# Kernel tuning notes

Hardware: AMD Instinct MI355X
Metric: run time of the kernel (lower is better)

Reference implementation:

```python
import jax, jax.numpy as jnp
import numpy as np

LAPLACE_SCALE = 0.5


def setup_inputs() -> dict:
    key = jax.random.key(0)
    k1, k2, k3 = jax.random.split(key, 3)
    B, M, D = 8, 512, 64
    return {
        "k": jax.random.normal(k1, (B, M, D), dtype=jnp.float32),
        "v": jax.random.normal(k2, (B, M, D), dtype=jnp.float32),
        "q": jax.random.normal(k3, (B, M, D), dtype=jnp.float32),
    }


def reference(k, v, q):
    # Laplace attention branch (faithful to original, including comparing k to v):
    # k_: [B,1,M,D], v_: [B,M,1,D] -> unnorm: [B,M,M]
    unnorm = jnp.abs((k[:, None, :, :] - v[:, :, None, :]) * LAPLACE_SCALE).sum(axis=-1)
    weights = jax.nn.softmax(unnorm, axis=-1)  # [B,M,M]
    rep = jnp.einsum('bik,bkj->bij', weights, v)  # [B,M,D]
    return rep
```

## Files before the change

kernel.cpp:

```cpp
#include <hip/hip_runtime.h>


typedef _Float16 h2 __attribute__((ext_vector_type(2)));

#if __has_builtin(__builtin_amdgcn_fdot2)
#define FDOT2(a, b, c) __builtin_amdgcn_fdot2((a), (b), (c), false)
#else
static __device__ inline float FDOT2(h2 a, h2 b, float c) {
    return c + (float)a.x * (float)b.x + (float)a.y * (float)b.y;
}
#endif

#if __has_builtin(__builtin_amdgcn_sad_u16)
#define SADU16(a, b, c) __builtin_amdgcn_sad_u16((a), (b), (c))
#else
static __device__ inline unsigned SADU16(unsigned a, unsigned b, unsigned c) {
    const unsigned al = a & 0xFFFFu, ah = a >> 16;
    const unsigned bl = b & 0xFFFFu, bh = b >> 16;
    const unsigned dl = al > bl ? al - bl : bl - al;
    const unsigned dh = ah > bh ? ah - bh : bh - ah;
    return c + dl + dh;
}
#endif

static __device__ inline unsigned pk16(float x, float y) {
    h2 h;
    h.x = (_Float16)x;
    h.y = (_Float16)y;
    return __builtin_bit_cast(unsigned, h);
}

static __device__ inline unsigned q16(float x) {
    return (unsigned)(x * 4096.0f + 32768.5f);
}

constexpr int B_ = 8, M_ = 512, D_ = 64;
constexpr int GRID1 = 8 * 16 * 8;
#define C2L  1.761099911e-4f
#define CFIX 67.0f

constexpr int OFF_KH  = 0;
constexpr int OFF_VH  = 2176;
constexpr int OFF_VJ2 = 3328;
constexpr int OFF_WH  = 5504;
constexpr int OFF_DEN = 6528;
constexpr int LDS_U   = 6656;

__global__ __launch_bounds__(256, 4)
void laplace_k1(const float* __restrict__ K, const float* __restrict__ V,
                unsigned* __restrict__ repH, float* __restrict__ den_part) {
    __shared__ __align__(16) unsigned lds[LDS_U];

    const int blk = blockIdx.x;
    const int b  = blk >> 7;
    const int it = (blk >> 3) & 15;
    const int jg = blk & 7;
    const int i0 = it * 32, j0 = jg * 64;

    const float* __restrict__ Kb = K + (size_t)b * (M_ * D_);
    const float* __restrict__ Vb = V + (size_t)b * (M_ * D_);

    const int t = threadIdx.x;

    {
        const int row = t >> 2, dq = t & 3;
        const float* kp = Kb + (size_t)(j0 + row) * D_ + dq * 16;
#pragma unroll
        for (int c = 0; c < 4; ++c) {
            const float4 q = *reinterpret_cast<const float4*>(kp + 4 * c);
            lds[OFF_KH + (dq * 8 + 2 * c + 0) * 68 + row] = q16(q.x) | (q16(q.y) << 16);
            lds[OFF_KH + (dq * 8 + 2 * c + 1) * 68 + row] = q16(q.z) | (q16(q.w) << 16);
        }
    }
    {
        const int row = t >> 3, dq = t & 7;
        const float* vp = Vb + (size_t)(i0 + row) * D_ + dq * 8;
        const float4 a  = *reinterpret_cast<const float4*>(vp);
        const float4 c4 = *reinterpret_cast<const float4*>(vp + 4);
        lds[OFF_VH + (dq * 4 + 0) * 36 + row] = q16(a.x)  | (q16(a.y)  << 16);
        lds[OFF_VH + (dq * 4 + 1) * 36 + row] = q16(a.z)  | (q16(a.w)  << 16);
        lds[OFF_VH + (dq * 4 + 2) * 36 + row] = q16(c4.x) | (q16(c4.y) << 16);
        lds[OFF_VH + (dq * 4 + 3) * 36 + row] = q16(c4.z) | (q16(c4.w) << 16);
    }
    {
        const int j2 = t >> 3;
        const int dc = (t & 7) * 8;
        const float* r0 = Vb + (size_t)(j0 + 2 * j2) * D_ + dc;
        const float* r1 = r0 + D_;
        unsigned o[8];
#pragma unroll
        for (int c = 0; c < 8; c += 4) {
            const float4 a  = *reinterpret_cast<const float4*>(r0 + c);
            const float4 bq = *reinterpret_cast<const float4*>(r1 + c);
            o[c + 0] = pk16(a.x, bq.x);
            o[c + 1] = pk16(a.y, bq.y);
            o[c + 2] = pk16(a.z, bq.z);
            o[c + 3] = pk16(a.w, bq.w);
        }
        *reinterpret_cast<uint4*>(&lds[OFF_VJ2 + j2 * 68 + dc]) =
            make_uint4(o[0], o[1], o[2], o[3]);
        *reinterpret_cast<uint4*>(&lds[OFF_VJ2 + j2 * 68 + dc + 4]) =
            make_uint4(o[4], o[5], o[6], o[7]);
    }
    __syncthreads();

    const int wv = t >> 6, lane = t & 63;
    const int ig = lane >> 2;
    const int jq = lane & 3;

    unsigned sacc[2][4];
#pragma unroll
    for (int a = 0; a < 2; ++a)
#pragma unroll
        for (int c = 0; c < 4; ++c) sacc[a][c] = 0u;

    const unsigned* pV = lds + OFF_VH + ig * 2;
    const unsigned* pK = lds + OFF_KH + wv * 16 + jq * 4;

#pragma unroll 8
    for (int d2 = 0; d2 < 32; ++d2) {
        const uint2 va = *reinterpret_cast<const uint2*>(pV + d2 * 36);
        const uint4 ka = *reinterpret_cast<const uint4*>(pK + d2 * 68);
        sacc[0][0] = SADU16(ka.x, va.x, sacc[0][0]);
        sacc[0][1] = SADU16(ka.y, va.x, sacc[0][1]);
        sacc[0][2] = SADU16(ka.z, va.x, sacc[0][2]);
        sacc[0][3] = SADU16(ka.w, va.x, sacc[0][3]);
        sacc[1][0] = SADU16(ka.x, va.y, sacc[1][0]);
        sacc[1][1] = SADU16(ka.y, va.y, sacc[1][1]);
        sacc[1][2] = SADU16(ka.z, va.y, sacc[1][2]);
        sacc[1][3] = SADU16(ka.w, va.y, sacc[1][3]);
    }

    float w[2][4], den[2];
#pragma unroll
    for (int a = 0; a < 2; ++a) {
        den[a] = 0.f;
#pragma unroll
        for (int c = 0; c < 4; ++c) {
            float e = exp2f((float)sacc[a][c] * C2L - CFIX);
            e = fminf(e, 60000.0f);
            w[a][c] = e;
            den[a] += e;
        }
        den[a] += __shfl_xor(den[a], 1);
        den[a] += __shfl_xor(den[a], 2);
    }
    float* dnl = reinterpret_cast<float*>(lds + OFF_DEN);
    if (jq == 0)
        *reinterpret_cast<float2*>(&dnl[wv * 32 + ig * 2]) = make_float2(den[0], den[1]);

    {
        unsigned* wH = lds + OFF_WH + wv * 256;
        const int j2 = jq * 2;
#pragma unroll
        for (int a = 0; a < 2; ++a) {
            wH[(j2 + 0) * 32 + ig * 2 + a] = pk16(w[a][0], w[a][1]);
            wH[(j2 + 1) * 32 + ig * 2 + a] = pk16(w[a][2], w[a][3]);
        }
    }

    const int ig3 = lane >> 3;
    const int dg  = lane & 7;

    float acc[4][8];
#pragma unroll
    for (int a = 0; a < 4; ++a)
#pragma unroll
        for (int c = 0; c < 8; ++c) acc[a][c] = 0.f;

    const unsigned* pW  = lds + OFF_WH + wv * 256 + ig3 * 4;
    const unsigned* pVJ = lds + OFF_VJ2 + (wv * 8) * 68 + dg * 8;

#pragma unroll
    for (int j2 = 0; j2 < 8; ++j2) {
        const uint4 wq = *reinterpret_cast<const uint4*>(pW + j2 * 32);
        const uint4 v0 = *reinterpret_cast<const uint4*>(pVJ + j2 * 68);
        const uint4 v1 = *reinterpret_cast<const uint4*>(pVJ + j2 * 68 + 4);
        const unsigned wA[4] = {wq.x, wq.y, wq.z, wq.w};
        const unsigned vA[8] = {v0.x, v0.y, v0.z, v0.w, v1.x, v1.y, v1.z, v1.w};
#pragma unroll
        for (int a = 0; a < 4; ++a) {
            const h2 wa = __builtin_bit_cast(h2, wA[a]);
#pragma unroll
            for (int c = 0; c < 8; ++c)
                acc[a][c] = FDOT2(wa, __builtin_bit_cast(h2, vA[c]), acc[a][c]);
        }
    }
    __syncthreads();

    {
        unsigned* cmb = lds + wv * 1024 + lane * 16;
#pragma unroll
        for (int a = 0; a < 4; ++a)
            *reinterpret_cast<uint4*>(cmb + a * 4) =
                make_uint4(pk16(acc[a][0], acc[a][1]), pk16(acc[a][2], acc[a][3]),
                           pk16(acc[a][4], acc[a][5]), pk16(acc[a][6], acc[a][7]));
    }
    __syncthreads();

    {
        const int i_  = t >> 3;
        const int dgr = t & 7;
        const int L   = ((i_ >> 2) << 3) + dgr;
        const int off = (i_ & 3) * 4;

        float x[4] = {0.f, 0.f, 0.f, 0.f}, y[4] = {0.f, 0.f, 0.f, 0.f};
#pragma unroll
        for (int wq = 0; wq < 4; ++wq) {
            const uint4 q = *reinterpret_cast<const uint4*>(lds + wq * 1024 + L * 16 + off);
            const unsigned qa[4] = {q.x, q.y, q.z, q.w};
#pragma unroll
            for (int c = 0; c < 4; ++c) {
                const h2 h = __builtin_bit_cast(h2, qa[c]);
                x[c] += (float)h.x;
                y[c] += (float)h.y;
            }
        }
        *reinterpret_cast<uint4*>(repH + (size_t)blk * 1024 + t * 4) =
            make_uint4(pk16(x[0], y[0]), pk16(x[1], y[1]),
                       pk16(x[2], y[2]), pk16(x[3], y[3]));

        if (t < 32)
            den_part[(size_t)blk * 32 + t] =
                (dnl[t] + dnl[32 + t]) + (dnl[64 + t] + dnl[96 + t]);
    }
}

__global__ __launch_bounds__(256)
void laplace_k2(const unsigned* __restrict__ repH,
                const float* __restrict__ den_part,
                float2* __restrict__ out2) {
    const int gid = blockIdx.x * 256 + threadIdx.x;
    const int b   = gid >> 14;
    const int i9  = (gid >> 5) & 511;
    const int d2  = gid & 31;
    const int it  = i9 >> 5, il = i9 & 31;

    const size_t base = (size_t)(b * 16 + it) * 8;

    float dsum = 0.f;
#pragma unroll
    for (int s = 0; s < 8; ++s) dsum += den_part[(base + s) * 32 + il];

    float ax = 0.f, ay = 0.f;
    const unsigned* rp = repH + base * 1024 + (size_t)il * 32 + d2;
#pragma unroll
    for (int s = 0; s < 8; ++s) {
        const h2 h = __builtin_bit_cast(h2, rp[(size_t)s * 1024]);
        ax += (float)h.x;
        ay += (float)h.y;
    }
    const float inv = 1.0f / dsum;
    out2[gid] = make_float2(ax * inv, ay * inv);
}

extern "C" void kernel_launch(void* const* d_in, const int* in_sizes, int n_in,
                              void* d_out, int out_size, void* d_ws, size_t ws_size,
                              hipStream_t stream) {
    const float* K = (const float*)d_in[0];
    const float* V = (const float*)d_in[1];

    unsigned* repH = (unsigned*)d_ws;
    float*    den  = (float*)((char*)d_ws + 4 * 1024 * 1024);

    laplace_k1<<<dim3(GRID1), dim3(256), 0, stream>>>(K, V, repH, den);
    laplace_k2<<<dim3(512), dim3(256), 0, stream>>>(repH, den, (float2*)d_out);
}
```

Measured before the change: 17.54 us.

## Split SAD reduction over D halves across lane groups with 4x4 register tiles

Restructures the L1-distance score loop so each half-wave covers half the feature dimension with a 4x4 row/column register tile instead of 2x4, then combines the partial sums with a cross-lane shuffle. Each wide LDS load now feeds more SAD ops, which improves reuse and halves the serial loop length. The exp, denominator and packed weight stores are redistributed so each half-wave handles two of the four columns, writing the weights as one vector store. In exchange it adds shuffles, uses more registers and changes the LDS access pattern.

```diff
diff --git a/kernel.cpp b/kernel.cpp
--- a/kernel.cpp
+++ b/kernel.cpp
@@ -105,58 +105,66 @@
     __syncthreads();
 
     const int wv = t >> 6, lane = t & 63;
-    const int ig = lane >> 2;
-    const int jq = lane & 3;
-
-    unsigned sacc[2][4];
-#pragma unroll
-    for (int a = 0; a < 2; ++a)
+    const int dh = lane >> 5;
+    const int l5 = lane & 31;
+    const int ig = l5 >> 2;
+    const int jq = l5 & 3;
+
+    unsigned sacc[4][4];
+#pragma unroll
+    for (int a = 0; a < 4; ++a)
 #pragma unroll
         for (int c = 0; c < 4; ++c) sacc[a][c] = 0u;
 
-    const unsigned* pV = lds + OFF_VH + ig * 2;
-    const unsigned* pK = lds + OFF_KH + wv * 16 + jq * 4;
-
-#pragma unroll 8
-    for (int d2 = 0; d2 < 32; ++d2) {
-        const uint2 va = *reinterpret_cast<const uint2*>(pV + d2 * 36);
+    const unsigned* pV = lds + OFF_VH + dh * (16 * 36) + ig * 4;
+    const unsigned* pK = lds + OFF_KH + dh * (16 * 68) + wv * 16 + jq * 4;
+
+#pragma unroll
+    for (int d2 = 0; d2 < 16; ++d2) {
+        const uint4 va = *reinterpret_cast<const uint4*>(pV + d2 * 36);
         const uint4 ka = *reinterpret_cast<const uint4*>(pK + d2 * 68);
-        sacc[0][0] = SADU16(ka.x, va.x, sacc[0][0]);
-        sacc[0][1] = SADU16(ka.y, va.x, sacc[0][1]);
-        sacc[0][2] = SADU16(ka.z, va.x, sacc[0][2]);
-        sacc[0][3] = SADU16(ka.w, va.x, sacc[0][3]);
-        sacc[1][0] = SADU16(ka.x, va.y, sacc[1][0]);
-        sacc[1][1] = SADU16(ka.y, va.y, sacc[1][1]);
-        sacc[1][2] = SADU16(ka.z, va.y, sacc[1][2]);
-        sacc[1][3] = SADU16(ka.w, va.y, sacc[1][3]);
-    }
-
-    float w[2][4], den[2];
-#pragma unroll
-    for (int a = 0; a < 2; ++a) {
-        den[a] = 0.f;
-#pragma unroll
-        for (int c = 0; c < 4; ++c) {
-            float e = exp2f((float)sacc[a][c] * C2L - CFIX);
-            e = fminf(e, 60000.0f);
-            w[a][c] = e;
-            den[a] += e;
-        }
-        den[a] += __shfl_xor(den[a], 1);
-        den[a] += __shfl_xor(den[a], 2);
+        const unsigned vaA[4] = {va.x, va.y, va.z, va.w};
+        const unsigned kaA[4] = {ka.x, ka.y, ka.z, ka.w};
+#pragma unroll
+        for (int a = 0; a < 4; ++a)
+#pragma unroll
+            for (int c = 0; c < 4; ++c)
+                sacc[a][c] = SADU16(kaA[c], vaA[a], sacc[a][c]);
+    }
+#pragma unroll
+    for (int a = 0; a < 4; ++a)
+#pragma unroll
+        for (int c = 0; c < 4; ++c)
+            sacc[a][c] += __shfl_xor(sacc[a][c], 32);
+
+    const int cc = dh * 2;
+    float w0[4], w1[4], denp[4];
+#pragma unroll
+    for (int a = 0; a < 4; ++a) {
+        float e0 = exp2f((float)sacc[a][cc + 0] * C2L - CFIX);
+        float e1 = exp2f((float)sacc[a][cc + 1] * C2L - CFIX);
+        e0 = fminf(e0, 60000.0f);
+        e1 = fminf(e1, 60000.0f);
+        w0[a] = e0;
+        w1[a] = e1;
+        denp[a] = e0 + e1;
+    }
+#pragma unroll
+    for (int a = 0; a < 4; ++a) {
+        denp[a] += __shfl_xor(denp[a], 32);
+        denp[a] += __shfl_xor(denp[a], 1);
+        denp[a] += __shfl_xor(denp[a], 2);
     }
     float* dnl = reinterpret_cast<float*>(lds + OFF_DEN);
-    if (jq == 0)
-        *reinterpret_cast<float2*>(&dnl[wv * 32 + ig * 2]) = make_float2(den[0], den[1]);
-
-    {
-        unsigned* wH = lds + OFF_WH + wv * 256;
-        const int j2 = jq * 2;
-#pragma unroll
-        for (int a = 0; a < 2; ++a) {
-            wH[(j2 + 0) * 32 + ig * 2 + a] = pk16(w[a][0], w[a][1]);
-            wH[(j2 + 1) * 32 + ig * 2 + a] = pk16(w[a][2], w[a][3]);
-        }
+    if (dh == 0 && jq == 0)
+        *reinterpret_cast<float4*>(&dnl[wv * 32 + ig * 4]) =
+            make_float4(denp[0], denp[1], denp[2], denp[3]);
+
+    {
+        const int j2 = jq * 2 + dh;
+        *reinterpret_cast<uint4*>(&lds[OFF_WH + wv * 256 + j2 * 32 + ig * 4]) =
+            make_uint4(pk16(w0[0], w1[0]), pk16(w0[1], w1[1]),
+                       pk16(w0[2], w1[2]), pk16(w0[3], w1[3]));
     }
 
     const int ig3 = lane >> 3;
```

Result: slower. 19.78 us (+12.8%).
